# Kernel tuning notes

Measured on AMD Instinct MI355X. Metric: run time of the kernel, lower is better.

The kernel has to match this reference:

```python
import jax, jax.numpy as jnp
import numpy as np

B, I, H = 16384, 512, 512


def _linear_params(key, out_dim, in_dim):
    kw, kb = jax.random.split(key)
    bound = 1.0 / np.sqrt(in_dim)
    W = jax.random.uniform(kw, (out_dim, in_dim), jnp.float32, -bound, bound)
    b = jax.random.uniform(kb, (out_dim,), jnp.float32, -bound, bound)
    return W, b


def setup_inputs() -> dict:
    key = jax.random.key(0)
    ks = jax.random.split(key, 12)
    x = jax.random.normal(ks[0], (B, I), jnp.float32)
    h_prev = jax.random.normal(ks[1], (B, H), jnp.float32)
    c_prev = jax.random.normal(ks[2], (B, H), jnp.float32)
    W_xi, b_xi = _linear_params(ks[3], H, I)
    W_hi, b_hi = _linear_params(ks[4], H, H)
    W_xf, b_xf = _linear_params(ks[5], H, I)
    W_hf, b_hf = _linear_params(ks[6], H, H)
    W_xc, b_xc = _linear_params(ks[7], H, I)
    W_hc, b_hc = _linear_params(ks[8], H, H)
    W_xo, b_xo = _linear_params(ks[9], H, I)
    W_ho, b_ho = _linear_params(ks[10], H, H)
    W_e, b_e = _linear_params(ks[11], H, I + H)
    return dict(x=x, h_prev=h_prev, c_prev=c_prev,
                W_xi=W_xi, b_xi=b_xi, W_hi=W_hi, b_hi=b_hi,
                W_xf=W_xf, b_xf=b_xf, W_hf=W_hf, b_hf=b_hf,
                W_xc=W_xc, b_xc=b_xc, W_hc=W_hc, b_hc=b_hc,
                W_xo=W_xo, b_xo=b_xo, W_ho=W_ho, b_ho=b_ho,
                W_e=W_e, b_e=b_e)


def reference(x, h_prev, c_prev,
              W_xi, b_xi, W_hi, b_hi,
              W_xf, b_xf, W_hf, b_hf,
              W_xc, b_xc, W_hc, b_hc,
              W_xo, b_xo, W_ho, b_ho,
              W_e, b_e):
    # Batch the 4 input-to-hidden projections into one GEMM and the 4
    # hidden-to-hidden projections into another (same math as 8 Linears).
    Wx = jnp.concatenate([W_xi, W_xf, W_xc, W_xo], axis=0)   # [4H, I]
    bx = jnp.concatenate([b_xi, b_xf, b_xc, b_xo], axis=0)   # [4H]
    Wh = jnp.concatenate([W_hi, W_hf, W_hc, W_ho], axis=0)   # [4H, H]
    bh = jnp.concatenate([b_hi, b_hf, b_hc, b_ho], axis=0)
    gates = (x @ Wx.T + bx) + (h_prev @ Wh.T + bh)            # [B, 4H]
    gi, gf, gc, go = jnp.split(gates, 4, axis=-1)
    i = jax.nn.sigmoid(gi)
    f = jax.nn.sigmoid(gf)
    g = jnp.tanh(gc)
    o = jax.nn.sigmoid(go)
    c = f * c_prev + i * g
    # exp gate: Linear on [x, h_prev] -> tanh -> exp; split W_e to avoid concat
    We_x, We_h = W_e[:, :x.shape[-1]], W_e[:, x.shape[-1]:]
    exp_factor = jnp.exp(jnp.tanh(x @ We_x.T + h_prev @ We_h.T + b_e))
    h = o * jnp.tanh(c) * exp_factor
    return (h, c)
```

## Files before the change

### kernel.cpp

```cpp
#include <hip/hip_runtime.h>
#include <stdint.h>

#define Bsz 16384
#define Hh  512
#define Kd  1024
#define BM  128
#define BNJ 32
#define BK  32
#define NT  32

#define BUFB 18432

typedef __attribute__((ext_vector_type(8))) short bf16x8;
typedef __attribute__((ext_vector_type(4))) float f32x4;
typedef __attribute__((ext_vector_type(8))) unsigned short u16x8;

__device__ __forceinline__ unsigned short f2bf(float f) {
    union { float f; unsigned u; } v; v.f = f;
    unsigned u = v.u;
    return (unsigned short)((u + 0x7fffu + ((u >> 16) & 1u)) >> 16);
}
__device__ __forceinline__ float fast_tanh(float x) {
    float e = __expf(2.f * x);
    return (e - 1.f) / (e + 1.f);
}
__device__ __forceinline__ float fast_sigmoid(float x) {
    return 1.f / (1.f + __expf(-x));
}

__global__ void pack_A(const float* __restrict__ x, const float* __restrict__ h,
                       unsigned short* __restrict__ A) {
    const long total = (long)Bsz * Kd / 8;
    for (long i = (long)blockIdx.x * blockDim.x + threadIdx.x; i < total;
         i += (long)gridDim.x * blockDim.x) {
        long row = i >> 7;
        int  col = ((int)(i & 127)) << 3;
        const float* src = (col < 512) ? (x + row * 512 + col)
                                       : (h + row * 512 + (col - 512));
        float4 f0 = *(const float4*)(src);
        float4 f1 = *(const float4*)(src + 4);
        u16x8 o;
        o[0]=f2bf(f0.x); o[1]=f2bf(f0.y); o[2]=f2bf(f0.z); o[3]=f2bf(f0.w);
        o[4]=f2bf(f1.x); o[5]=f2bf(f1.y); o[6]=f2bf(f1.z); o[7]=f2bf(f1.w);
        *(u16x8*)(A + (i << 3)) = o;
    }
}

__global__ void pack_B(const float* __restrict__ Wxi, const float* __restrict__ Whi,
                       const float* __restrict__ Wxf, const float* __restrict__ Whf,
                       const float* __restrict__ Wxc, const float* __restrict__ Whc,
                       const float* __restrict__ Wxo, const float* __restrict__ Who,
                       const float* __restrict__ We,
                       const float* __restrict__ bxi, const float* __restrict__ bhi,
                       const float* __restrict__ bxf, const float* __restrict__ bhf,
                       const float* __restrict__ bxc, const float* __restrict__ bhc,
                       const float* __restrict__ bxo, const float* __restrict__ bho,
                       const float* __restrict__ be,
                       unsigned short* __restrict__ Bp, float* __restrict__ bias) {
    const long id = (long)blockIdx.x * blockDim.x + threadIdx.x;
    if (id < 327680) {
        int blk = (int)(id >> 6);
        int l   = (int)(id & 63);
        int kh  = blk & 1;
        int kt  = (blk >> 1) & 15;
        int rest = blk >> 5;
        int g    = rest % 5;
        int jgrp = rest / 5;
        int j  = jgrp * 16 + (l & 15);
        int k0 = kt * 64 + kh * 32 + ((l >> 4) << 3);
        const float* src;
        if (g == 4) {
            src = We + (long)j * 1024 + k0;
        } else {
            const float* Wx = (g == 0) ? Wxi : (g == 1) ? Wxf : (g == 2) ? Wxc : Wxo;
            const float* Wh = (g == 0) ? Whi : (g == 1) ? Whf : (g == 2) ? Whc : Who;
            src = (k0 < 512) ? (Wx + (long)j * 512 + k0)
                             : (Wh + (long)j * 512 + (k0 - 512));
        }
        float4 f0 = *(const float4*)(src);
        float4 f1 = *(const float4*)(src + 4);
        u16x8 o;
        o[0]=f2bf(f0.x); o[1]=f2bf(f0.y); o[2]=f2bf(f0.z); o[3]=f2bf(f0.w);
        o[4]=f2bf(f1.x); o[5]=f2bf(f1.y); o[6]=f2bf(f1.z); o[7]=f2bf(f1.w);
        *(u16x8*)(Bp + (long)blk * 512 + l * 8) = o;
    }
    if (id < 2560) {
        int row = (int)id;
        int g = row >> 9, j = row & 511;
        float b;
        if (g == 4) b = be[j];
        else {
            const float* bx = (g == 0) ? bxi : (g == 1) ? bxf : (g == 2) ? bxc : bxo;
            const float* bh = (g == 0) ? bhi : (g == 1) ? bhf : (g == 2) ? bhc : bho;
            b = bx[j] + bh[j];
        }
        bias[row] = b;
    }
}

#define GL16(g, l) __builtin_amdgcn_global_load_lds( \
    (const __attribute__((address_space(1))) unsigned int*)(g), \
    (__attribute__((address_space(3))) unsigned int*)(l), 16, 0, 0)

#define VM0()      asm volatile("s_waitcnt vmcnt(0)" ::: "memory")
#define LGKM0()    asm volatile("s_waitcnt lgkmcnt(0)" ::: "memory")
#define BARRIER()  asm volatile("s_barrier" ::: "memory")
#define SCHED0()   __builtin_amdgcn_sched_barrier(0)

#define MF(a, b, c) __builtin_amdgcn_mfma_f32_16x16x32_bf16(a, b, c, 0, 0, 0)

#define RD9(RBO) do { \
    afA[0] = *(const bf16x8*)(aP + (RBO) + 0 * 1024); \
    afA[1] = *(const bf16x8*)(aP + (RBO) + 1 * 1024); \
    afA[2] = *(const bf16x8*)(aP + (RBO) + 2 * 1024); \
    afA[3] = *(const bf16x8*)(aP + (RBO) + 3 * 1024); \
    bq[0]  = *(const bf16x8*)(bP + (RBO) + 0 * 1024); \
    bq[1]  = *(const bf16x8*)(bP + (RBO) + 1 * 1024); \
    bq[2]  = *(const bf16x8*)(bP + (RBO) + 2 * 1024); \
    bq[3]  = *(const bf16x8*)(bP + (RBO) + 3 * 1024); \
    bq[4]  = *(const bf16x8*)(bP + (RBO) + 4 * 1024); \
} while (0)

#define MFMA20() do { \
    __builtin_amdgcn_s_setprio(1); \
    _Pragma("unroll") \
    for (int g_ = 0; g_ < 5; ++g_) { \
        acc[g_][0] = MF(afA[0], bq[g_], acc[g_][0]); \
        acc[g_][1] = MF(afA[1], bq[g_], acc[g_][1]); \
        acc[g_][2] = MF(afA[2], bq[g_], acc[g_][2]); \
        acc[g_][3] = MF(afA[3], bq[g_], acc[g_][3]); \
    } \
    __builtin_amdgcn_s_setprio(0); \
} while (0)

#define SG5(SO, T) do { \
    GL16(asg0 + (T) * 32,  lds_raw + (SO) + adst0); \
    GL16(asg1 + (T) * 32,  lds_raw + (SO) + adst1); \
    GL16(bsg0 + (T) * 512, lds_raw + (SO) + bdo0); \
    GL16(bsg1 + (T) * 512, lds_raw + (SO) + bdo1); \
    GL16(bsg2 + (T) * 512, lds_raw + (SO) + bdo2); \
} while (0)

#define TILE(RBO, SBO, T, STG, SYNC) do { \
    if (STG) SG5(SBO, (T) + 1); \
    RD9(RBO); \
    LGKM0(); SCHED0(); \
    MFMA20(); \
    if (SYNC) { VM0(); BARRIER(); } \
} while (0)

__global__ __launch_bounds__(256, 3)
void xlstm_gemm(const unsigned short* __restrict__ A,
                const unsigned short* __restrict__ Bp,
                const float* __restrict__ bias,
                const float* __restrict__ c_prev,
                float* __restrict__ out) {
    __shared__ __align__(16) unsigned char lds_raw[2 * BUFB];

    const int tid  = threadIdx.x;
    const int wid  = tid >> 6;
    const int lane = tid & 63;
    const int wm   = wid >> 1;
    const int wj   = wid & 1;
    const int fr   = lane & 15;
    const int q    = lane >> 4;

    const int orig = blockIdx.x;
    const int wg   = (orig & 7) * 256 + (orig >> 3);
    const int mblk = wg >> 4;
    const int jblk = wg & 15;
    const long brow = (long)mblk * BM;
    const int  bcol = jblk * BNJ;

    f32x4 acc[5][4];
#pragma unroll
    for (int g = 0; g < 5; ++g)
#pragma unroll
        for (int m = 0; m < 4; ++m)
#pragma unroll
            for (int r = 0; r < 4; ++r) acc[g][m][r] = 0.f;

    bf16x8 afA[4];
    bf16x8 bq[5];

    const unsigned char* aP = lds_raw + wm * 4096 + fr * 64
                              + ((q ^ ((fr >> 1) & 3)) << 4);
    const unsigned char* bP = lds_raw + 8192 + wj * 5120 + lane * 16;

    const int arow = tid >> 2;
    const unsigned short* asg0 = A + (brow + arow) * 1024L
                                   + (((tid & 3) ^ ((arow >> 1) & 3)) << 3);
    const unsigned short* asg1 = asg0 + 65536;
    const int adst0 = tid * 16;
    const int adst1 = tid * 16 + 4096;
    const unsigned short *bsg0, *bsg1, *bsg2;
    int bdo0, bdo1, bdo2;
#define BSTG_INIT(i) do { \
    int u_ = wid + 4 * (i); if (u_ >= 10) u_ -= 10; \
    int jl_ = u_ / 5; int g_ = u_ - 5 * jl_; \
    bsg##i = Bp + (long)(jblk * 2 + jl_) * 81920 + g_ * 16384 + lane * 8; \
    bdo##i = 8192 + u_ * 1024 + lane * 16; \
} while (0)
    BSTG_INIT(0); BSTG_INIT(1); BSTG_INIT(2);
#undef BSTG_INIT

    SG5(0, 0);
    VM0();
    BARRIER();

    for (int t = 0; t < 30; t += 2) {
        TILE(0,    BUFB, t,     1, 1);
        TILE(BUFB, 0,    t + 1, 1, 1);
    }
    TILE(0,    BUFB, 30, 1, 1);
    TILE(BUFB, 0,    31, 0, 0);

    const int j = bcol + wj * 16 + fr;
    const float bi_ = bias[j];
    const float bf_ = bias[512 + j];
    const float bc_ = bias[1024 + j];
    const float bo_ = bias[1536 + j];
    const float be_ = bias[2048 + j];
    const long mbase = brow + wm * 64 + (q << 2);
#pragma unroll
    for (int m = 0; m < 4; ++m) {
#pragma unroll
        for (int r = 0; r < 4; ++r) {
            long row = mbase + m * 16 + r;
            float gi = acc[0][m][r] + bi_;
            float gf = acc[1][m][r] + bf_;
            float gc = acc[2][m][r] + bc_;
            float go = acc[3][m][r] + bo_;
            float ge = acc[4][m][r] + be_;
            float iv = fast_sigmoid(gi);
            float fv = fast_sigmoid(gf);
            float gv = fast_tanh(gc);
            float ov = fast_sigmoid(go);
            float ef = __expf(fast_tanh(ge));
            float cp = c_prev[row * 512 + j];
            float cv = fv * cp + iv * gv;
            float hv = ov * fast_tanh(cv) * ef;
            out[row * 512 + j] = hv;
            out[(long)Bsz * 512 + row * 512 + j] = cv;
        }
    }
}

extern "C" void kernel_launch(void* const* d_in, const int* in_sizes, int n_in,
                              void* d_out, int out_size, void* d_ws, size_t ws_size,
                              hipStream_t stream) {
    const float* x      = (const float*)d_in[0];
    const float* h_prev = (const float*)d_in[1];
    const float* c_prev = (const float*)d_in[2];
    const float* Wxi = (const float*)d_in[3];
    const float* bxi = (const float*)d_in[4];
    const float* Whi = (const float*)d_in[5];
    const float* bhi = (const float*)d_in[6];
    const float* Wxf = (const float*)d_in[7];
    const float* bxf = (const float*)d_in[8];
    const float* Whf = (const float*)d_in[9];
    const float* bhf = (const float*)d_in[10];
    const float* Wxc = (const float*)d_in[11];
    const float* bxc = (const float*)d_in[12];
    const float* Whc = (const float*)d_in[13];
    const float* bhc = (const float*)d_in[14];
    const float* Wxo = (const float*)d_in[15];
    const float* bxo = (const float*)d_in[16];
    const float* Who = (const float*)d_in[17];
    const float* bho = (const float*)d_in[18];
    const float* We  = (const float*)d_in[19];
    const float* be  = (const float*)d_in[20];

    unsigned short* Abf  = (unsigned short*)d_ws;
    unsigned short* Bp   = (unsigned short*)((char*)d_ws + 33554432);
    float*          bias = (float*)((char*)d_ws + 33554432 + 5242880);

    pack_A<<<2048, 256, 0, stream>>>(x, h_prev, Abf);
    pack_B<<<1280, 256, 0, stream>>>(Wxi, Whi, Wxf, Whf, Wxc, Whc, Wxo, Who, We,
                                     bxi, bhi, bxf, bhf, bxc, bhc, bxo, bho, be,
                                     Bp, bias);
    xlstm_gemm<<<2048, 256, 0, stream>>>(Abf, Bp, bias, c_prev, (float*)d_out);
}
```

Baseline: 121.2 us.

## Switch GEMM to 32x32x16 MFMA with fragment-ordered prepacked A and B

Replaces the 16x16x32 bf16 MFMA tiling with 32x32x16 MFMA. Each wave now owns 32 rows by 32 columns across the five gates instead of a 64x16 tile. The pack kernels are rewritten to store A and B already in the MFMA fragment order, so LDS reads become simple lane-linear loads with no swizzle. The explicit lgkmcnt wait and sched barrier are dropped, leaving the compiler to schedule LDS reads against the MFMAs. The intent is fewer MFMA instructions and LDS reads per FLOP, at the cost of relying on compiler scheduling and possible LDS bank conflicts from the unswizzled layout.

```diff
diff --git a/kernel.cpp b/kernel.cpp
--- a/kernel.cpp
+++ b/kernel.cpp
@@ -6,13 +6,12 @@
 #define Kd  1024
 #define BM  128
 #define BNJ 32
-#define BK  32
 #define NT  32
 
 #define BUFB 18432
 
 typedef __attribute__((ext_vector_type(8))) short bf16x8;
-typedef __attribute__((ext_vector_type(4))) float f32x4;
+typedef __attribute__((ext_vector_type(16))) float f32x16;
 typedef __attribute__((ext_vector_type(8))) unsigned short u16x8;
 
 __device__ __forceinline__ unsigned short f2bf(float f) {
@@ -33,10 +32,15 @@
     const long total = (long)Bsz * Kd / 8;
     for (long i = (long)blockIdx.x * blockDim.x + threadIdx.x; i < total;
          i += (long)gridDim.x * blockDim.x) {
-        long row = i >> 7;
-        int  col = ((int)(i & 127)) << 3;
-        const float* src = (col < 512) ? (x + row * 512 + col)
-                                       : (h + row * 512 + (col - 512));
+        int  l    = (int)(i & 63);
+        long blk  = i >> 6;
+        int  u    = (int)(blk & 3);
+        int  kt   = (int)((blk >> 2) & 63);
+        long mblk = blk >> 8;
+        long row  = mblk * 128 + u * 32 + (l & 31);
+        int  k0   = kt * 16 + ((l >> 5) << 3);
+        const float* src = (k0 < 512) ? (x + row * 512 + k0)
+                                      : (h + row * 512 + (k0 - 512));
         float4 f0 = *(const float4*)(src);
         float4 f1 = *(const float4*)(src + 4);
         u16x8 o;
@@ -61,13 +65,12 @@
     if (id < 327680) {
         int blk = (int)(id >> 6);
         int l   = (int)(id & 63);
-        int kh  = blk & 1;
-        int kt  = (blk >> 1) & 15;
-        int rest = blk >> 5;
+        int kt  = blk & 63;
+        int rest = blk >> 6;
         int g    = rest % 5;
         int jgrp = rest / 5;
-        int j  = jgrp * 16 + (l & 15);
-        int k0 = kt * 64 + kh * 32 + ((l >> 4) << 3);
+        int j  = jgrp * 32 + (l & 31);
+        int k0 = kt * 16 + ((l >> 5) << 3);
         const float* src;
         if (g == 4) {
             src = We + (long)j * 1024 + k0;
@@ -103,54 +106,64 @@
     (__attribute__((address_space(3))) unsigned int*)(l), 16, 0, 0)
 
 #define VM0()      asm volatile("s_waitcnt vmcnt(0)" ::: "memory")
-#define LGKM0()    asm volatile("s_waitcnt lgkmcnt(0)" ::: "memory")
 #define BARRIER()  asm volatile("s_barrier" ::: "memory")
-#define SCHED0()   __builtin_amdgcn_sched_barrier(0)
-
-#define MF(a, b, c) __builtin_amdgcn_mfma_f32_16x16x32_bf16(a, b, c, 0, 0, 0)
-
-#define RD9(RBO) do { \
-    afA[0] = *(const bf16x8*)(aP + (RBO) + 0 * 1024); \
-    afA[1] = *(const bf16x8*)(aP + (RBO) + 1 * 1024); \
-    afA[2] = *(const bf16x8*)(aP + (RBO) + 2 * 1024); \
-    afA[3] = *(const bf16x8*)(aP + (RBO) + 3 * 1024); \
-    bq[0]  = *(const bf16x8*)(bP + (RBO) + 0 * 1024); \
-    bq[1]  = *(const bf16x8*)(bP + (RBO) + 1 * 1024); \
-    bq[2]  = *(const bf16x8*)(bP + (RBO) + 2 * 1024); \
-    bq[3]  = *(const bf16x8*)(bP + (RBO) + 3 * 1024); \
-    bq[4]  = *(const bf16x8*)(bP + (RBO) + 4 * 1024); \
-} while (0)
-
-#define MFMA20() do { \
+
+#define MF32(a, b, c) __builtin_amdgcn_mfma_f32_32x32x16_bf16(a, b, c, 0, 0, 0)
+
+#define RDK0(RBO) do { \
+    af0 = *(const bf16x8*)(aRP + (RBO)); \
+    b0  = *(const bf16x8*)(bRP + (RBO) + 0 * 1024); \
+    b1  = *(const bf16x8*)(bRP + (RBO) + 1 * 1024); \
+    b2  = *(const bf16x8*)(bRP + (RBO) + 2 * 1024); \
+    b3  = *(const bf16x8*)(bRP + (RBO) + 3 * 1024); \
+    b4  = *(const bf16x8*)(bRP + (RBO) + 4 * 1024); \
+} while (0)
+#define RDK1(RBO) do { \
+    af1 = *(const bf16x8*)(aRP + (RBO) + 4096); \
+    b5  = *(const bf16x8*)(bRP + (RBO) + 5120 + 0 * 1024); \
+    b6  = *(const bf16x8*)(bRP + (RBO) + 5120 + 1 * 1024); \
+    b7  = *(const bf16x8*)(bRP + (RBO) + 5120 + 2 * 1024); \
+    b8  = *(const bf16x8*)(bRP + (RBO) + 5120 + 3 * 1024); \
+    b9  = *(const bf16x8*)(bRP + (RBO) + 5120 + 4 * 1024); \
+} while (0)
+
+#define MFMA5A() do { \
     __builtin_amdgcn_s_setprio(1); \
-    _Pragma("unroll") \
-    for (int g_ = 0; g_ < 5; ++g_) { \
-        acc[g_][0] = MF(afA[0], bq[g_], acc[g_][0]); \
-        acc[g_][1] = MF(afA[1], bq[g_], acc[g_][1]); \
-        acc[g_][2] = MF(afA[2], bq[g_], acc[g_][2]); \
-        acc[g_][3] = MF(afA[3], bq[g_], acc[g_][3]); \
-    } \
+    acc[0] = MF32(af0, b0, acc[0]); \
+    acc[1] = MF32(af0, b1, acc[1]); \
+    acc[2] = MF32(af0, b2, acc[2]); \
+    acc[3] = MF32(af0, b3, acc[3]); \
+    acc[4] = MF32(af0, b4, acc[4]); \
     __builtin_amdgcn_s_setprio(0); \
 } while (0)
+#define MFMA5B() do { \
+    __builtin_amdgcn_s_setprio(1); \
+    acc[0] = MF32(af1, b5, acc[0]); \
+    acc[1] = MF32(af1, b6, acc[1]); \
+    acc[2] = MF32(af1, b7, acc[2]); \
+    acc[3] = MF32(af1, b8, acc[3]); \
+    acc[4] = MF32(af1, b9, acc[4]); \
+    __builtin_amdgcn_s_setprio(0); \
+} while (0)
 
 #define SG5(SO, T) do { \
-    GL16(asg0 + (T) * 32,  lds_raw + (SO) + adst0); \
-    GL16(asg1 + (T) * 32,  lds_raw + (SO) + adst1); \
-    GL16(bsg0 + (T) * 512, lds_raw + (SO) + bdo0); \
-    GL16(bsg1 + (T) * 512, lds_raw + (SO) + bdo1); \
-    GL16(bsg2 + (T) * 512, lds_raw + (SO) + bdo2); \
+    GL16(asg0 + (T) * 4096, lds_raw + (SO) + adst0); \
+    GL16(asg1 + (T) * 4096, lds_raw + (SO) + adst1); \
+    GL16(bsg0 + (T) * 1024, lds_raw + (SO) + bdo0); \
+    GL16(bsg1 + (T) * 1024, lds_raw + (SO) + bdo1); \
+    GL16(bsg2 + (T) * 1024, lds_raw + (SO) + bdo2); \
 } while (0)
 
 #define TILE(RBO, SBO, T, STG, SYNC) do { \
     if (STG) SG5(SBO, (T) + 1); \
-    RD9(RBO); \
-    LGKM0(); SCHED0(); \
-    MFMA20(); \
+    RDK0(RBO); RDK1(RBO); \
+    MFMA5A(); \
+    MFMA5B(); \
     if (SYNC) { VM0(); BARRIER(); } \
 } while (0)
 
 __global__ __launch_bounds__(256, 3)
-void xlstm_gemm(const unsigned short* __restrict__ A,
+void xlstm_gemm(const unsigned short* __restrict__ Apk,
                 const unsigned short* __restrict__ Bp,
                 const float* __restrict__ bias,
                 const float* __restrict__ c_prev,
@@ -160,10 +173,9 @@
     const int tid  = threadIdx.x;
     const int wid  = tid >> 6;
     const int lane = tid & 63;
-    const int wm   = wid >> 1;
-    const int wj   = wid & 1;
-    const int fr   = lane & 15;
-    const int q    = lane >> 4;
+    const int wm   = wid;
+    const int jl   = lane & 31;
+    const int q5   = lane >> 5;
 
     const int orig = blockIdx.x;
     const int wg   = (orig & 7) * 256 + (orig >> 3);
@@ -172,33 +184,27 @@
     const long brow = (long)mblk * BM;
     const int  bcol = jblk * BNJ;
 
-    f32x4 acc[5][4];
+    f32x16 acc[5];
 #pragma unroll
     for (int g = 0; g < 5; ++g)
 #pragma unroll
-        for (int m = 0; m < 4; ++m)
-#pragma unroll
-            for (int r = 0; r < 4; ++r) acc[g][m][r] = 0.f;
-
-    bf16x8 afA[4];
-    bf16x8 bq[5];
-
-    const unsigned char* aP = lds_raw + wm * 4096 + fr * 64
-                              + ((q ^ ((fr >> 1) & 3)) << 4);
-    const unsigned char* bP = lds_raw + 8192 + wj * 5120 + lane * 16;
-
-    const int arow = tid >> 2;
-    const unsigned short* asg0 = A + (brow + arow) * 1024L
-                                   + (((tid & 3) ^ ((arow >> 1) & 3)) << 3);
-    const unsigned short* asg1 = asg0 + 65536;
+        for (int r = 0; r < 16; ++r) acc[g][r] = 0.f;
+
+    bf16x8 af0, af1, b0, b1, b2, b3, b4, b5, b6, b7, b8, b9;
+
+    const unsigned char* aRP = lds_raw + wm * 1024 + lane * 16;
+    const unsigned char* bRP = lds_raw + 8192 + lane * 16;
+
+    const unsigned short* asg0 = Apk + (long)mblk * 131072 + tid * 8;
+    const unsigned short* asg1 = asg0 + 2048;
     const int adst0 = tid * 16;
-    const int adst1 = tid * 16 + 4096;
+    const int adst1 = 4096 + tid * 16;
     const unsigned short *bsg0, *bsg1, *bsg2;
     int bdo0, bdo1, bdo2;
 #define BSTG_INIT(i) do { \
     int u_ = wid + 4 * (i); if (u_ >= 10) u_ -= 10; \
-    int jl_ = u_ / 5; int g_ = u_ - 5 * jl_; \
-    bsg##i = Bp + (long)(jblk * 2 + jl_) * 81920 + g_ * 16384 + lane * 8; \
+    int ks_ = u_ / 5; int g_ = u_ - 5 * ks_; \
+    bsg##i = Bp + ((long)(jblk * 5 + g_) * 64 + ks_) * 512 + lane * 8; \
     bdo##i = 8192 + u_ * 1024 + lane * 16; \
 } while (0)
     BSTG_INIT(0); BSTG_INIT(1); BSTG_INIT(2);
@@ -215,34 +221,31 @@
     TILE(0,    BUFB, 30, 1, 1);
     TILE(BUFB, 0,    31, 0, 0);
 
-    const int j = bcol + wj * 16 + fr;
+    const int j = bcol + jl;
     const float bi_ = bias[j];
     const float bf_ = bias[512 + j];
     const float bc_ = bias[1024 + j];
     const float bo_ = bias[1536 + j];
     const float be_ = bias[2048 + j];
-    const long mbase = brow + wm * 64 + (q << 2);
+    const long rbase = brow + wm * 32 + 4 * q5;
 #pragma unroll
-    for (int m = 0; m < 4; ++m) {
-#pragma unroll
-        for (int r = 0; r < 4; ++r) {
-            long row = mbase + m * 16 + r;
-            float gi = acc[0][m][r] + bi_;
-            float gf = acc[1][m][r] + bf_;
-            float gc = acc[2][m][r] + bc_;
-            float go = acc[3][m][r] + bo_;
-            float ge = acc[4][m][r] + be_;
-            float iv = fast_sigmoid(gi);
-            float fv = fast_sigmoid(gf);
-            float gv = fast_tanh(gc);
-            float ov = fast_sigmoid(go);
-            float ef = __expf(fast_tanh(ge));
-            float cp = c_prev[row * 512 + j];
-            float cv = fv * cp + iv * gv;
-            float hv = ov * fast_tanh(cv) * ef;
-            out[row * 512 + j] = hv;
-            out[(long)Bsz * 512 + row * 512 + j] = cv;
-        }
+    for (int r = 0; r < 16; ++r) {
+        long row = rbase + (r & 3) + 8 * (r >> 2);
+        float gi = acc[0][r] + bi_;
+        float gf = acc[1][r] + bf_;
+        float gc = acc[2][r] + bc_;
+        float go = acc[3][r] + bo_;
+        float ge = acc[4][r] + be_;
+        float iv = fast_sigmoid(gi);
+        float fv = fast_sigmoid(gf);
+        float gv = fast_tanh(gc);
+        float ov = fast_sigmoid(go);
+        float ef = __expf(fast_tanh(ge));
+        float cp = c_prev[row * 512 + j];
+        float cv = fv * cp + iv * gv;
+        float hv = ov * fast_tanh(cv) * ef;
+        out[row * 512 + j] = hv;
+        out[(long)Bsz * 512 + row * 512 + j] = cv;
     }
 }
 
```

Measured after the change: 141.4 us. 16.7% more time.
